# Kernel optimization log

Measured on AMD Instinct MI355X. Metric: run time of the kernel, lower is better.

Reference implementation:

```python
import jax, jax.numpy as jnp
import numpy as np

N, NFEAT, NHID, OUT, E, P = 50000, 256, 128, 64, 800000, 3
WALK_STEPS, LAMBDA_RW = 13, 0.2


def spmm(row, col, val, x):
    # sparse (N,N) @ dense (N,d) via gather + segment-sum over destination rows
    return jax.ops.segment_sum(val[:, None] * x[col], row, num_segments=N)


def telu(x):
    return x * jnp.tanh(jnp.exp(x))


def setup_inputs() -> dict:
    key = jax.random.key(0)
    ks = jax.random.split(key, 24)
    s = 0.05
    inp = {
        'feature': jax.random.normal(ks[0], (N, NFEAT), jnp.float32),
        'edge_index': jax.random.randint(ks[1], (P, 2, E), 0, N, jnp.int64),
        'edge_val': jax.random.uniform(ks[2], (P, E), jnp.float32) / 16.0,
        'spec_w1': jax.random.normal(ks[3], (P, NFEAT, NHID)) * s,
        'spec_b1': jax.random.normal(ks[4], (P, NHID)) * s,
        'spec_w2': jax.random.normal(ks[5], (P, NHID, OUT)) * s,
        'spec_b2': jax.random.normal(ks[6], (P, OUT)) * s,
        'shared_w1': jax.random.normal(ks[7], (NFEAT, NHID)) * s,
        'shared_b1': jax.random.normal(ks[8], (NHID,)) * s,
        'shared_w2': jax.random.normal(ks[9], (NHID, OUT)) * s,
        'shared_b2': jax.random.normal(ks[10], (OUT,)) * s,
        'weight_b': jax.random.normal(ks[11], (P, 1)) * s,
        'tau': jnp.float32(0.5),
        'mlp_w1': jax.random.normal(ks[12], (OUT * P, NHID)) * s,
        'mlp_b1': jax.random.normal(ks[13], (NHID,)) * s,
        'mlp_w2': jax.random.normal(ks[14], (NHID, OUT)) * s,
        'mlp_b2': jax.random.normal(ks[15], (OUT,)) * s,
        'raw_w1': jax.random.normal(ks[16], (NFEAT, OUT)) * s,
        'raw_b1': jax.random.normal(ks[17], (OUT,)) * s,
        'raw_w2': jax.random.normal(ks[18], (OUT, OUT)) * s,
        'raw_b2': jax.random.normal(ks[19], (OUT,)) * s,
        'proj_w': jax.random.normal(ks[20], (OUT * 4, OUT)) * s,
        'proj_b': jax.random.normal(ks[21], (OUT,)) * s,
    }
    return inp


def reference(feature, edge_index, edge_val, spec_w1, spec_b1, spec_w2, spec_b2,
              shared_w1, shared_b1, shared_w2, shared_b2, weight_b, tau,
              mlp_w1, mlp_b1, mlp_w2, mlp_b2, raw_w1, raw_b1, raw_w2, raw_b2,
              proj_w, proj_b):
    rows = [edge_index[i, 0] for i in range(P)]
    cols = [edge_index[i, 1] for i in range(P)]
    vals = [edge_val[i] for i in range(P)]

    def gc(x, w, b, i):
        return spmm(rows[i], cols[i], vals[i], x @ w) + b

    # path-specific two-layer GCNs (dropout in eval mode = identity)
    specific = []
    for i in range(P):
        h1 = telu(gc(feature, spec_w1[i], spec_b1[i], i))
        specific.append(gc(h1, spec_w2[i], spec_b2[i], i))
    spec_stack = jnp.stack(specific, axis=0)  # (P, N, OUT)

    # shared GCN applied per path
    shared = []
    for i in range(P):
        h1 = telu(gc(feature, shared_w1, shared_b1, i))
        shared.append(gc(h1, shared_w2, shared_b2, i))
    shared_stack = jnp.stack(shared, axis=0)
    H_sh = jnp.mean(shared_stack, axis=0)

    # markov-enhanced path attention
    summaries = []
    for s in specific:
        mean_pool = s.mean(axis=0)
        max_pool = s.max(axis=0)
        p = jax.nn.softmax(s, axis=0)
        entropy = -jnp.sum(p * jnp.log(p + 1e-6), axis=0)
        summaries.append(jnp.concatenate([mean_pool, max_pool, entropy], axis=-1))
    ps = jnp.stack(summaries, axis=0)  # (P, 3*OUT)
    sim = (ps @ ps.T) / (jnp.sqrt(jnp.float32(3 * OUT)) * tau)
    T = jax.nn.softmax(sim, axis=1)
    pi0 = jax.nn.softmax(weight_b.squeeze(-1), axis=0)
    pi = pi0
    for _ in range(WALK_STEPS):
        pi = LAMBDA_RW * pi0 + (1.0 - LAMBDA_RW) * (pi @ T)
    W_tilde = pi[:, None]  # beta dropout is identity in eval mode

    # collaborative MLP on concatenated specific features
    concat_sp = jnp.concatenate(specific, axis=1)  # (N, P*OUT)
    H_col = jax.nn.relu(concat_sp @ mlp_w1 + mlp_b1) @ mlp_w2 + mlp_b2

    # attention-fused specific features
    wprob = jax.nn.softmax(W_tilde, axis=0)[:, 0]  # (P,)
    H_sp_fused = jnp.einsum('pnd,p->nd', spec_stack, wprob)

    # raw path on merged adjacency: final_A = sum_i W_tilde[i] * A_i (applied lazily)
    w = W_tilde[:, 0]

    def merged_spmm(x):
        acc = jnp.zeros((N, x.shape[1]), x.dtype)
        for i in range(P):
            acc = acc + w[i] * spmm(rows[i], cols[i], vals[i], x)
        return acc

    U1 = merged_spmm(feature @ raw_w1) + raw_b1
    U2 = merged_spmm(U1 @ raw_w2) + raw_b2
    H_raw = (U1 + U2) / 2.0

    all_feat = jnp.concatenate([H_sp_fused, H_sh, H_col, H_raw], axis=1)
    out = all_feat @ proj_w + proj_b
    return (out, spec_stack, shared_stack, H_col, H_raw)
```

## Files before the change

kernel.cpp:

```cpp
#include <hip/hip_runtime.h>
#include <hip/hip_bf16.h>
#include <math.h>

#define NN 50000
#define NFEAT 256
#define NHID 128
#define OUTD 64
#define NE 800000
#define NP 3
#define NCH 64
#define RC 782
#define NSB 196
#define NNR (NN + 1)
#define NBUK 256
#define BROWS 196
#define BCAP 4096
#define EPB 8192

typedef __hip_bfloat16 bf16;
typedef __attribute__((ext_vector_type(8))) short short8;
typedef __attribute__((ext_vector_type(4))) short short4v;
typedef __attribute__((ext_vector_type(4))) float f32x4;
typedef unsigned long long u64;

static inline int cdiv(long a, long b) { return (int)((a + b - 1) / b); }

__device__ __forceinline__ short f2bf(float x) {
    unsigned u = __builtin_bit_cast(unsigned, x);
    unsigned r = (u + 0x7FFFu + ((u >> 16) & 1u)) >> 16;
    return (short)r;
}
__device__ __forceinline__ float bf2f(short b) {
    unsigned u = ((unsigned)(unsigned short)b) << 16;
    return __builtin_bit_cast(float, u);
}

__device__ __forceinline__ float telu_f(float x) {
    float e = __expf(x);
    float t = __expf(-2.0f * e);
    return x * (1.0f - t) / (1.0f + t);
}

__device__ __forceinline__ void ld8(const float* __restrict__ p, float v[8]) {
    float4 a = *reinterpret_cast<const float4*>(p);
    float4 b = *reinterpret_cast<const float4*>(p + 4);
    v[0] = a.x; v[1] = a.y; v[2] = a.z; v[3] = a.w;
    v[4] = b.x; v[5] = b.y; v[6] = b.z; v[7] = b.w;
}

__device__ __forceinline__ void store4(float* p, const float o[4]) {
    *reinterpret_cast<float4*>(p) = make_float4(o[0], o[1], o[2], o[3]);
}
__device__ __forceinline__ void store4(bf16* p, const float o[4]) {
    short4v u;
    u[0] = f2bf(o[0]); u[1] = f2bf(o[1]); u[2] = f2bf(o[2]); u[3] = f2bf(o[3]);
    *reinterpret_cast<short4v*>(p) = u;
}

__global__ void transpose_split(const float* __restrict__ src, bf16* __restrict__ dh,
                                bf16* __restrict__ dl, int K, int M, long total) {
    long idx = (long)blockIdx.x * blockDim.x + threadIdx.x;
    if (idx >= total) return;
    long pm = idx / K;
    int k = (int)(idx - pm * K);
    long p = pm / M;
    int m = (int)(pm - p * M);
    float v = src[(p * K + k) * M + m];
    short hb = f2bf(v);
    short lb = f2bf(v - bf2f(hb));
    reinterpret_cast<short*>(dh)[idx] = hb;
    reinterpret_cast<short*>(dl)[idx] = lb;
}

template <int K, int M, int MODE, int ACT, typename OT>
__global__ __launch_bounds__(256) void gemm_mfma(
    const float* __restrict__ A, const bf16* __restrict__ Bh, const bf16* __restrict__ Bl,
    const float* __restrict__ bias, OT* __restrict__ out, int nrows,
    const float* __restrict__ wvec, const float* __restrict__ s1,
    const float* __restrict__ s2, const float* __restrict__ s3) {
    constexpr int MC = M / 16;
    __shared__ short AsH[64 * 32];
    __shared__ short AsL[64 * 32];

    int t = threadIdx.x;
    int n0 = blockIdx.x * 64;
    int w = t >> 6;
    int l = t & 63;
    int lr = l & 15, lq = l >> 4;

    float w0 = 0.f, w1 = 0.f, w2 = 0.f;
    if (MODE == 2) { w0 = wvec[3]; w1 = wvec[4]; w2 = wvec[5]; }

    f32x4 acc[MC];
#pragma unroll
    for (int i = 0; i < MC; ++i) {
        f32x4 z = {0.f, 0.f, 0.f, 0.f};
        acc[i] = z;
    }

    int sr = t >> 2, sc = t & 3;
    int gn_s = n0 + sr;
    int wslot = (sc ^ ((sr >> 2) & 3)) << 3;
    short* wpH = &AsH[sr * 32 + wslot];
    short* wpL = &AsL[sr * 32 + wslot];

    int rrow = (w << 4) + lr;
    int roff = rrow * 32 + ((lq ^ ((rrow >> 2) & 3)) << 3);
    const short* rpH = &AsH[roff];
    const short* rpL = &AsL[roff];

    const short* Bhs = reinterpret_cast<const short*>(Bh);
    const short* Bls = reinterpret_cast<const short*>(Bl);

    auto loadA = [&](int k0, float v[8]) {
        if (gn_s >= nrows) {
#pragma unroll
            for (int j = 0; j < 8; ++j) v[j] = 0.f;
            return;
        }
        if (MODE == 0) {
            ld8(A + (long)gn_s * K + k0 + sc * 8, v);
        } else if (MODE == 1) {
            int plane = k0 >> 6;
            int d = (k0 & 63) + sc * 8;
            ld8(A + ((long)plane * NN + gn_s) * OUTD + d, v);
        } else {
            int seg = k0 >> 6;
            int d = (k0 & 63) + sc * 8;
            if (seg == 0) {
                float x0[8], x1[8], x2[8];
                ld8(A + ((long)0 * NN + gn_s) * OUTD + d, x0);
                ld8(A + ((long)1 * NN + gn_s) * OUTD + d, x1);
                ld8(A + ((long)2 * NN + gn_s) * OUTD + d, x2);
#pragma unroll
                for (int j = 0; j < 8; ++j) v[j] = w0 * x0[j] + w1 * x1[j] + w2 * x2[j];
            } else if (seg == 1) {
                float x0[8], x1[8], x2[8];
                ld8(s1 + ((long)0 * NN + gn_s) * OUTD + d, x0);
                ld8(s1 + ((long)1 * NN + gn_s) * OUTD + d, x1);
                ld8(s1 + ((long)2 * NN + gn_s) * OUTD + d, x2);
#pragma unroll
                for (int j = 0; j < 8; ++j) v[j] = (x0[j] + x1[j] + x2[j]) * (1.0f / 3.0f);
            } else if (seg == 2) {
                ld8(s2 + (long)gn_s * OUTD + d, v);
            } else {
                ld8(s3 + (long)gn_s * OUTD + d, v);
            }
        }
    };

    float v[8];
    loadA(0, v);
    for (int k0 = 0; k0 < K; k0 += 32) {
        short8 ah, al;
#pragma unroll
        for (int j = 0; j < 8; ++j) {
            short hb = f2bf(v[j]);
            ah[j] = hb;
            al[j] = f2bf(v[j] - bf2f(hb));
        }
        __syncthreads();
        *reinterpret_cast<short8*>(wpH) = ah;
        *reinterpret_cast<short8*>(wpL) = al;
        __syncthreads();
        if (k0 + 32 < K) loadA(k0 + 32, v);
        short8 fah = *reinterpret_cast<const short8*>(rpH);
        short8 fal = *reinterpret_cast<const short8*>(rpL);
#pragma unroll
        for (int m = 0; m < MC; ++m) {
            long wb = (long)(m * 16 + lr) * K + k0 + (lq << 3);
            short8 bh = *reinterpret_cast<const short8*>(Bhs + wb);
            short8 bl = *reinterpret_cast<const short8*>(Bls + wb);
            acc[m] = __builtin_amdgcn_mfma_f32_16x16x32_bf16(bh, fah, acc[m], 0, 0, 0);
            acc[m] = __builtin_amdgcn_mfma_f32_16x16x32_bf16(bl, fah, acc[m], 0, 0, 0);
            acc[m] = __builtin_amdgcn_mfma_f32_16x16x32_bf16(bh, fal, acc[m], 0, 0, 0);
        }
    }

    int gn = n0 + (w << 4) + lr;
    if (gn < nrows) {
#pragma unroll
        for (int m = 0; m < MC; ++m) {
            int mb = m * 16 + (lq << 2);
            float o[4];
#pragma unroll
            for (int r = 0; r < 4; ++r) {
                o[r] = acc[m][r] + (bias ? bias[mb + r] : 0.f);
                if (ACT == 2) o[r] = fmaxf(o[r], 0.f);
            }
            store4(&out[(long)gn * M + mb], o);
        }
    }
}

__global__ void hist_all(const int* __restrict__ ei, int* __restrict__ cnt) {
    int p = blockIdx.y;
    int e = blockIdx.x * blockDim.x + threadIdx.x;
    if (e >= NE) return;
    int r = ei[((long)p * 2) * NE + e];
    atomicAdd(&cnt[(long)p * NN + r], 1);
}

__global__ void scan_pass1(const int* __restrict__ cnt, int* __restrict__ bsum) {
    int p = blockIdx.y, b = blockIdx.x, t = threadIdx.x;
    int idx = b * 256 + t;
    int v = (idx < NN) ? cnt[(long)p * NN + idx] : 0;
    __shared__ int sh[256];
    sh[t] = v;
    __syncthreads();
    for (int off = 128; off > 0; off >>= 1) {
        if (t < off) sh[t] += sh[t + off];
        __syncthreads();
    }
    if (t == 0) bsum[p * NSB + b] = sh[0];
}

__global__ void scan_pass2(const int* __restrict__ bsum, int* __restrict__ boff) {
    int p = blockIdx.x, t = threadIdx.x;
    int v = (t < NSB) ? bsum[p * NSB + t] : 0;
    __shared__ int sh[256];
    sh[t] = v;
    __syncthreads();
    for (int off = 1; off < 256; off <<= 1) {
        int tmp = (t >= off) ? sh[t - off] : 0;
        __syncthreads();
        sh[t] += tmp;
        __syncthreads();
    }
    if (t < NSB) boff[p * NSB + t] = sh[t] - v;
}

__global__ void scan_pass3(const int* __restrict__ cnt, const int* __restrict__ boff,
                           int* __restrict__ rowptr) {
    int p = blockIdx.y, b = blockIdx.x, t = threadIdx.x;
    int idx = b * 256 + t;
    int v = (idx < NN) ? cnt[(long)p * NN + idx] : 0;
    __shared__ int sh[256];
    sh[t] = v;
    __syncthreads();
    for (int off = 1; off < 256; off <<= 1) {
        int tmp = (t >= off) ? sh[t - off] : 0;
        __syncthreads();
        sh[t] += tmp;
        __syncthreads();
    }
    int rp = boff[p * NSB + b] + sh[t] - v;
    if (idx < NN) rowptr[(long)p * NNR + idx] = rp;
    if (idx == NN - 1) rowptr[(long)p * NNR + NN] = rp + v;
}

__global__ __launch_bounds__(256) void bucket_append2(
    const int* __restrict__ ei, const float* __restrict__ ev,
    int* __restrict__ bcnt, int2* __restrict__ bbuf) {
    int p = blockIdx.y;
    int t = threadIdx.x;
    long e0 = (long)blockIdx.x * EPB;
    const int* rs = ei + ((long)p * 2) * NE;
    const int* cs = rs + NE;
    const float* vs = ev + (long)p * NE;
    __shared__ int lcnt[NBUK];
    __shared__ int lbase[NBUK];
    for (int b = t; b < NBUK; b += 256) lcnt[b] = 0;
    __syncthreads();
    for (int i = t; i < EPB; i += 256) {
        long e = e0 + i;
        if (e < NE) atomicAdd(&lcnt[rs[e] / BROWS], 1);
    }
    __syncthreads();
    for (int b = t; b < NBUK; b += 256) {
        int c = lcnt[b];
        lbase[b] = (c > 0) ? atomicAdd(&bcnt[p * NBUK + b], c) : 0;
        lcnt[b] = 0;
    }
    __syncthreads();
    for (int i = t; i < EPB; i += 256) {
        long e = e0 + i;
        if (e >= NE) continue;
        int r = rs[e];
        int b = r / BROWS;
        int off = atomicAdd(&lcnt[b], 1);
        int pos = lbase[b] + off;
        int meta = ((r - b * BROWS) << 16) | cs[e];
        bbuf[((long)p * NBUK + b) * BCAP + pos] = make_int2(meta, __float_as_int(vs[e]));
    }
}

__global__ __launch_bounds__(256) void bucket_scatter2(
    const int* __restrict__ bcnt, const int2* __restrict__ bbuf,
    const int* __restrict__ rowptr, int2* __restrict__ csr) {
    int b = blockIdx.x, p = blockIdx.y;
    int t = threadIdx.x;
    int row0 = b * BROWS;
    int nrows = min(BROWS, NN - row0);
    __shared__ int cur[BROWS];
    for (int i = t; i < nrows; i += 256) cur[i] = rowptr[(long)p * NNR + row0 + i];
    __syncthreads();
    int cntb = bcnt[p * NBUK + b];
    const int2* buf = bbuf + ((long)p * NBUK + b) * BCAP;
    int2* csrp = csr + (long)p * NE;
    for (int i = t; i < cntb; i += 256) {
        int2 ent = buf[i];
        int row_off = ent.x >> 16;
        int col = ent.x & 0xFFFF;
        int pos = atomicAdd(&cur[row_off], 1);
        csrp[pos] = make_int2(col, ent.y);
    }
}

template <int M, int ACT, int RPB>
__global__ void spmm_dual(const int* __restrict__ rowptr, const int2* __restrict__ csr,
                          const bf16* __restrict__ Ya, const bf16* __restrict__ Yb,
                          const float* __restrict__ biasA, const float* __restrict__ biasB,
                          float* __restrict__ outA, float* __restrict__ outB) {
    constexpr int TPR = M / 2;
    int t = threadIdx.x;
    int n = blockIdx.x * RPB + t / TPR;
    int hs = t % TPR;
    int h = hs * 2;
    if (n >= NN) return;
    int e0 = rowptr[n], e1 = rowptr[n + 1];
    float aAl = biasA[h], aAh = biasA[h + 1];
    float aBl = biasB[h], aBh = biasB[h + 1];
    const unsigned* Ua = reinterpret_cast<const unsigned*>(Ya);
    const unsigned* Ub = reinterpret_cast<const unsigned*>(Yb);
    int e = e0;
    for (; e + 3 < e1; e += 4) {
        int2 p0 = csr[e], p1 = csr[e + 1], p2 = csr[e + 2], p3 = csr[e + 3];
        unsigned a0 = Ua[(long)p0.x * TPR + hs], a1 = Ua[(long)p1.x * TPR + hs];
        unsigned a2 = Ua[(long)p2.x * TPR + hs], a3 = Ua[(long)p3.x * TPR + hs];
        unsigned b0 = Ub[(long)p0.x * TPR + hs], b1 = Ub[(long)p1.x * TPR + hs];
        unsigned b2 = Ub[(long)p2.x * TPR + hs], b3 = Ub[(long)p3.x * TPR + hs];
        float v0 = __int_as_float(p0.y), v1 = __int_as_float(p1.y);
        float v2 = __int_as_float(p2.y), v3 = __int_as_float(p3.y);
        aAl += v0 * bf2f((short)a0) + v1 * bf2f((short)a1) + v2 * bf2f((short)a2) + v3 * bf2f((short)a3);
        aAh += v0 * bf2f((short)(a0 >> 16)) + v1 * bf2f((short)(a1 >> 16)) +
               v2 * bf2f((short)(a2 >> 16)) + v3 * bf2f((short)(a3 >> 16));
        aBl += v0 * bf2f((short)b0) + v1 * bf2f((short)b1) + v2 * bf2f((short)b2) + v3 * bf2f((short)b3);
        aBh += v0 * bf2f((short)(b0 >> 16)) + v1 * bf2f((short)(b1 >> 16)) +
               v2 * bf2f((short)(b2 >> 16)) + v3 * bf2f((short)(b3 >> 16));
    }
    for (; e < e1; ++e) {
        int2 pe = csr[e];
        float v = __int_as_float(pe.y);
        unsigned a = Ua[(long)pe.x * TPR + hs];
        unsigned b = Ub[(long)pe.x * TPR + hs];
        aAl += v * bf2f((short)a);
        aAh += v * bf2f((short)(a >> 16));
        aBl += v * bf2f((short)b);
        aBh += v * bf2f((short)(b >> 16));
    }
    if (ACT == 1) {
        aAl = telu_f(aAl); aAh = telu_f(aAh);
        aBl = telu_f(aBl); aBh = telu_f(aBh);
    }
    *reinterpret_cast<float2*>(&outA[(long)n * M + h]) = make_float2(aAl, aAh);
    *reinterpret_cast<float2*>(&outB[(long)n * M + h]) = make_float2(aBl, aBh);
}

__global__ void spmm_merged(const int* __restrict__ rp0, const int2* __restrict__ cs0,
                            const int* __restrict__ rp1, const int2* __restrict__ cs1,
                            const int* __restrict__ rp2, const int2* __restrict__ cs2,
                            const bf16* __restrict__ Y, const float* __restrict__ wvec,
                            const float* __restrict__ bias, float* __restrict__ out) {
    constexpr int TPR = 32;
    int t = threadIdx.x;
    int n = blockIdx.x * 2 + t / TPR;
    int hs = t % TPR;
    int h = hs * 2;
    if (n >= NN) return;
    const int* rps[3] = {rp0, rp1, rp2};
    const int2* css[3] = {cs0, cs1, cs2};
    const unsigned* U = reinterpret_cast<const unsigned*>(Y);
    float al = 0.f, ah = 0.f;
#pragma unroll
    for (int p = 0; p < 3; ++p) {
        const int2* cs = css[p];
        int e0 = rps[p][n], e1 = rps[p][n + 1];
        float sl = 0.f, sh = 0.f;
        int e = e0;
        for (; e + 3 < e1; e += 4) {
            int2 p0 = cs[e], p1 = cs[e + 1], p2 = cs[e + 2], p3 = cs[e + 3];
            unsigned y0 = U[(long)p0.x * TPR + hs], y1 = U[(long)p1.x * TPR + hs];
            unsigned y2 = U[(long)p2.x * TPR + hs], y3 = U[(long)p3.x * TPR + hs];
            float v0 = __int_as_float(p0.y), v1 = __int_as_float(p1.y);
            float v2 = __int_as_float(p2.y), v3 = __int_as_float(p3.y);
            sl += v0 * bf2f((short)y0) + v1 * bf2f((short)y1) + v2 * bf2f((short)y2) + v3 * bf2f((short)y3);
            sh += v0 * bf2f((short)(y0 >> 16)) + v1 * bf2f((short)(y1 >> 16)) +
                  v2 * bf2f((short)(y2 >> 16)) + v3 * bf2f((short)(y3 >> 16));
        }
        for (; e < e1; ++e) {
            int2 pe = cs[e];
            unsigned y = U[(long)pe.x * TPR + hs];
            float v = __int_as_float(pe.y);
            sl += v * bf2f((short)y);
            sh += v * bf2f((short)(y >> 16));
        }
        float wv = wvec[p];
        al += wv * sl;
        ah += wv * sh;
    }
    *reinterpret_cast<float2*>(&out[(long)n * OUTD + h]) =
        make_float2(al + bias[h], ah + bias[h + 1]);
}

__global__ void colsum_passA(const float* __restrict__ spec, float* __restrict__ pmax,
                             float* __restrict__ psum, float* __restrict__ pexp) {
    int p = blockIdx.y, c = blockIdx.x;
    int t = threadIdx.x;
    int d = t & 63, rg = t >> 6;
    const float* base = spec + (long)p * NN * OUTD;
    int r0 = c * RC, r1 = min(r0 + RC, NN);
    float m = -INFINITY, s = 0.f, e = 0.f;
    for (int r = r0 + rg; r < r1; r += 4) {
        float v = base[(long)r * OUTD + d];
        s += v;
        if (v > m) { e = e * __expf(m - v) + 1.0f; m = v; }
        else e += __expf(v - m);
    }
    __shared__ float rm[256], rs[256], re[256];
    rm[t] = m; rs[t] = s; re[t] = e;
    __syncthreads();
    for (int off = 128; off >= 64; off >>= 1) {
        if (t < off) {
            float m2 = fmaxf(rm[t], rm[t + off]);
            re[t] = re[t] * __expf(rm[t] - m2) + re[t + off] * __expf(rm[t + off] - m2);
            rm[t] = m2;
            rs[t] = rs[t] + rs[t + off];
        }
        __syncthreads();
    }
    if (t < 64) {
        long idx = ((long)p * 64 + t) * NCH + c;
        pmax[idx] = rm[t]; psum[idx] = rs[t]; pexp[idx] = re[t];
    }
}

__global__ void colsum_reduceB(const float* __restrict__ pmax, const float* __restrict__ psum,
                               const float* __restrict__ pexp, float* __restrict__ ps,
                               float* __restrict__ zbuf) {
    int b = blockIdx.x;
    int p = b >> 6, d = b & 63;
    int t = threadIdx.x;
    long idx = (long)b * NCH + t;
    float m = pmax[idx], s = psum[idx], e = pexp[idx];
    for (int off = 32; off > 0; off >>= 1) {
        float m2 = fmaxf(m, __shfl_xor(m, off));
        e = e * __expf(m - m2) + __shfl_xor(e, off) * __expf(__shfl_xor(m, off) - m2);
        m = m2;
        s += __shfl_xor(s, off);
    }
    if (t == 0) {
        ps[p * 192 + d] = s / (float)NN;
        ps[p * 192 + 64 + d] = m;
        zbuf[b] = e;
    }
}

__global__ void colsum_passC(const float* __restrict__ spec, const float* __restrict__ ps,
                             const float* __restrict__ zbuf, float* __restrict__ pent) {
    int p = blockIdx.y, c = blockIdx.x;
    int t = threadIdx.x;
    int d = t & 63, rg = t >> 6;
    const float* base = spec + (long)p * NN * OUTD;
    float gm = ps[p * 192 + 64 + d];
    float zinv = 1.0f / zbuf[p * 64 + d];
    int r0 = c * RC, r1 = min(r0 + RC, NN);
    float ent = 0.f;
    for (int r = r0 + rg; r < r1; r += 4) {
        float v = base[(long)r * OUTD + d];
        float pv = __expf(v - gm) * zinv;
        ent -= pv * __logf(pv + 1e-6f);
    }
    __shared__ float rd[256];
    rd[t] = ent;
    __syncthreads();
    for (int off = 128; off >= 64; off >>= 1) {
        if (t < off) rd[t] += rd[t + off];
        __syncthreads();
    }
    if (t < 64) pent[((long)p * 64 + t) * NCH + c] = rd[t];
}

__global__ void colsum_reduceD(const float* __restrict__ pent, float* __restrict__ ps) {
    int b = blockIdx.x;
    int p = b >> 6, d = b & 63;
    int t = threadIdx.x;
    float e = pent[(long)b * NCH + t];
    for (int off = 32; off > 0; off >>= 1) e += __shfl_xor(e, off);
    if (t == 0) ps[p * 192 + 128 + d] = e;
}

__global__ void walk_kernel(const float* __restrict__ ps, const float* __restrict__ weight_b,
                            const float* __restrict__ tau_p, float* __restrict__ wout) {
    if (threadIdx.x != 0 || blockIdx.x != 0) return;
    float sim[3][3];
    float inv = 1.0f / (sqrtf(192.0f) * tau_p[0]);
    for (int i = 0; i < 3; ++i)
        for (int j = 0; j < 3; ++j) {
            float dotv = 0.f;
            for (int k = 0; k < 192; ++k) dotv += ps[i * 192 + k] * ps[j * 192 + k];
            sim[i][j] = dotv * inv;
        }
    float T[3][3];
    for (int i = 0; i < 3; ++i) {
        float m = fmaxf(sim[i][0], fmaxf(sim[i][1], sim[i][2]));
        float e0 = expf(sim[i][0] - m), e1 = expf(sim[i][1] - m), e2 = expf(sim[i][2] - m);
        float s = e0 + e1 + e2;
        T[i][0] = e0 / s; T[i][1] = e1 / s; T[i][2] = e2 / s;
    }
    float b0 = weight_b[0], b1 = weight_b[1], b2 = weight_b[2];
    float m = fmaxf(b0, fmaxf(b1, b2));
    float e0 = expf(b0 - m), e1 = expf(b1 - m), e2 = expf(b2 - m);
    float s = e0 + e1 + e2;
    float pi0[3] = {e0 / s, e1 / s, e2 / s};
    float pi[3] = {pi0[0], pi0[1], pi0[2]};
    for (int it = 0; it < 13; ++it) {
        float n0 = pi[0] * T[0][0] + pi[1] * T[1][0] + pi[2] * T[2][0];
        float n1 = pi[0] * T[0][1] + pi[1] * T[1][1] + pi[2] * T[2][1];
        float n2 = pi[0] * T[0][2] + pi[1] * T[1][2] + pi[2] * T[2][2];
        pi[0] = 0.2f * pi0[0] + 0.8f * n0;
        pi[1] = 0.2f * pi0[1] + 0.8f * n1;
        pi[2] = 0.2f * pi0[2] + 0.8f * n2;
    }
    wout[0] = pi[0]; wout[1] = pi[1]; wout[2] = pi[2];
    float mm = fmaxf(pi[0], fmaxf(pi[1], pi[2]));
    float f0 = expf(pi[0] - mm), f1 = expf(pi[1] - mm), f2 = expf(pi[2] - mm);
    float fs = f0 + f1 + f2;
    wout[3] = f0 / fs; wout[4] = f1 / fs; wout[5] = f2 / fs;
}

__global__ void hraw_final(const float* __restrict__ U1, float* __restrict__ Hraw) {
    long i = (long)blockIdx.x * blockDim.x + threadIdx.x;
    if (i >= (long)NN * OUTD) return;
    Hraw[i] = 0.5f * (U1[i] + Hraw[i]);
}

extern "C" void kernel_launch(void* const* d_in, const int* in_sizes, int n_in,
                              void* d_out, int out_size, void* d_ws, size_t ws_size,
                              hipStream_t stream) {
    const float* feature   = (const float*)d_in[0];
    const int*   edge_index= (const int*)d_in[1];
    const float* edge_val  = (const float*)d_in[2];
    const float* spec_w1   = (const float*)d_in[3];
    const float* spec_b1   = (const float*)d_in[4];
    const float* spec_w2   = (const float*)d_in[5];
    const float* spec_b2   = (const float*)d_in[6];
    const float* shared_w1 = (const float*)d_in[7];
    const float* shared_b1 = (const float*)d_in[8];
    const float* shared_w2 = (const float*)d_in[9];
    const float* shared_b2 = (const float*)d_in[10];
    const float* weight_b  = (const float*)d_in[11];
    const float* tau       = (const float*)d_in[12];
    const float* mlp_w1    = (const float*)d_in[13];
    const float* mlp_b1    = (const float*)d_in[14];
    const float* mlp_w2    = (const float*)d_in[15];
    const float* mlp_b2    = (const float*)d_in[16];
    const float* raw_w1    = (const float*)d_in[17];
    const float* raw_b1    = (const float*)d_in[18];
    const float* raw_w2    = (const float*)d_in[19];
    const float* raw_b2    = (const float*)d_in[20];
    const float* proj_w    = (const float*)d_in[21];
    const float* proj_b    = (const float*)d_in[22];

    float* out        = (float*)d_out;
    float* spec_stack = out + (long)NN * OUTD;
    float* shr_stack  = spec_stack + 3L * NN * OUTD;
    float* Hcol       = out + 7L * NN * OUTD;
    float* Hraw       = out + 8L * NN * OUTD;

    char* wp = (char*)d_ws;
    bf16* XWsp = (bf16*)wp; wp += (long)NN * 128 * sizeof(bf16);
    bf16* XWsh = (bf16*)wp; wp += (long)NN * 128 * sizeof(bf16);
    bf16* Bsp  = (bf16*)wp; wp += (long)NN * OUTD * sizeof(bf16);
    bf16* Bsh  = (bf16*)wp; wp += (long)NN * OUTD * sizeof(bf16);
    float* h1sp = (float*)wp; wp += (long)NN * 128 * sizeof(float);
    float* h1sh = (float*)wp; wp += (long)NN * 128 * sizeof(float);
    float* psBuf = (float*)wp; wp += 1024 * sizeof(float);
    float* wBuf  = (float*)wp; wp += 64 * sizeof(float);
    float* zBuf  = (float*)wp; wp += 256 * sizeof(float);
    float* pMax  = (float*)wp; wp += (long)3 * 64 * NCH * sizeof(float);
    float* pSum  = (float*)wp; wp += (long)3 * 64 * NCH * sizeof(float);
    float* pExp  = (float*)wp; wp += (long)3 * 64 * NCH * sizeof(float);
    float* pEnt  = (float*)wp; wp += (long)3 * 64 * NCH * sizeof(float);
    int2* csr_all = (int2*)wp;  wp += (long)NP * NE * sizeof(int2);
    int*  rowptr_all = (int*)wp; wp += (long)NP * NNR * sizeof(int) + 64;
    int* cnt    = (int*)wp; wp += (long)NP * NN * sizeof(int);
    int* bsum   = (int*)wp; wp += (long)NP * NSB * sizeof(int);
    int* boff   = (int*)wp; wp += (long)NP * NSB * sizeof(int);
    int* bcnt   = (int*)wp; wp += (long)NP * NBUK * sizeof(int);
    int2* bbuf  = (int2*)wp; wp += (long)NP * NBUK * BCAP * sizeof(int2);
    bf16* w1sp_h = (bf16*)wp; wp += 3L * 256 * 128 * sizeof(bf16);
    bf16* w1sp_l = (bf16*)wp; wp += 3L * 256 * 128 * sizeof(bf16);
    bf16* w1sh_h = (bf16*)wp; wp += 256L * 128 * sizeof(bf16);
    bf16* w1sh_l = (bf16*)wp; wp += 256L * 128 * sizeof(bf16);
    bf16* w2sp_h = (bf16*)wp; wp += 3L * 128 * 64 * sizeof(bf16);
    bf16* w2sp_l = (bf16*)wp; wp += 3L * 128 * 64 * sizeof(bf16);
    bf16* w2sh_h = (bf16*)wp; wp += 128L * 64 * sizeof(bf16);
    bf16* w2sh_l = (bf16*)wp; wp += 128L * 64 * sizeof(bf16);
    bf16* mlp1_h = (bf16*)wp; wp += 192L * 128 * sizeof(bf16);
    bf16* mlp1_l = (bf16*)wp; wp += 192L * 128 * sizeof(bf16);
    bf16* mlp2_h = (bf16*)wp; wp += 128L * 64 * sizeof(bf16);
    bf16* mlp2_l = (bf16*)wp; wp += 128L * 64 * sizeof(bf16);
    bf16* raw1_h = (bf16*)wp; wp += 256L * 64 * sizeof(bf16);
    bf16* raw1_l = (bf16*)wp; wp += 256L * 64 * sizeof(bf16);
    bf16* raw2_h = (bf16*)wp; wp += 64L * 64 * sizeof(bf16);
    bf16* raw2_l = (bf16*)wp; wp += 64L * 64 * sizeof(bf16);
    bf16* proj_h = (bf16*)wp; wp += 256L * 64 * sizeof(bf16);
    bf16* proj_l = (bf16*)wp; wp += 256L * 64 * sizeof(bf16);

    int* rowptr[NP]; int2* csr[NP];
    for (int p = 0; p < NP; ++p) {
        rowptr[p] = rowptr_all + (long)p * NNR;
        csr[p]    = csr_all + (long)p * NE;
    }

    const int TB = 256;
    int g_rows = cdiv(NN, 64);

    transpose_split<<<cdiv(3L * 256 * 128, TB), TB, 0, stream>>>(spec_w1, w1sp_h, w1sp_l, 256, 128, 3L * 256 * 128);
    transpose_split<<<cdiv(256L * 128, TB), TB, 0, stream>>>(shared_w1, w1sh_h, w1sh_l, 256, 128, 256L * 128);
    transpose_split<<<cdiv(3L * 128 * 64, TB), TB, 0, stream>>>(spec_w2, w2sp_h, w2sp_l, 128, 64, 3L * 128 * 64);
    transpose_split<<<cdiv(128L * 64, TB), TB, 0, stream>>>(shared_w2, w2sh_h, w2sh_l, 128, 64, 128L * 64);
    transpose_split<<<cdiv(192L * 128, TB), TB, 0, stream>>>(mlp_w1, mlp1_h, mlp1_l, 192, 128, 192L * 128);
    transpose_split<<<cdiv(128L * 64, TB), TB, 0, stream>>>(mlp_w2, mlp2_h, mlp2_l, 128, 64, 128L * 64);
    transpose_split<<<cdiv(256L * 64, TB), TB, 0, stream>>>(raw_w1, raw1_h, raw1_l, 256, 64, 256L * 64);
    transpose_split<<<cdiv(64L * 64, TB), TB, 0, stream>>>(raw_w2, raw2_h, raw2_l, 64, 64, 64L * 64);
    transpose_split<<<cdiv(256L * 64, TB), TB, 0, stream>>>(proj_w, proj_h, proj_l, 256, 64, 256L * 64);

    hipMemsetAsync(cnt, 0, (long)NP * NN * sizeof(int), stream);
    hipMemsetAsync(bcnt, 0, (long)NP * NBUK * sizeof(int), stream);
    {
        dim3 gE(cdiv(NE, TB), NP);
        hist_all<<<gE, TB, 0, stream>>>(edge_index, cnt);
        dim3 gA(cdiv(NE, EPB), NP);
        bucket_append2<<<gA, 256, 0, stream>>>(edge_index, edge_val, bcnt, bbuf);
        dim3 gS(NSB, NP);
        scan_pass1<<<gS, 256, 0, stream>>>(cnt, bsum);
        scan_pass2<<<NP, 256, 0, stream>>>(bsum, boff);
        scan_pass3<<<gS, 256, 0, stream>>>(cnt, boff, rowptr_all);
        dim3 gB(NBUK, NP);
        bucket_scatter2<<<gB, 256, 0, stream>>>(bcnt, bbuf, rowptr_all, csr_all);
    }

    gemm_mfma<256, 128, 0, 0, bf16><<<g_rows, 256, 0, stream>>>(
        feature, w1sh_h, w1sh_l, nullptr, XWsh, NN, nullptr, nullptr, nullptr, nullptr);

    for (int p = 0; p < NP; ++p) {
        gemm_mfma<256, 128, 0, 0, bf16><<<g_rows, 256, 0, stream>>>(
            feature, w1sp_h + (long)p * 256 * 128, w1sp_l + (long)p * 256 * 128,
            nullptr, XWsp, NN, nullptr, nullptr, nullptr, nullptr);
        spmm_dual<128, 1, 1><<<NN, 64, 0, stream>>>(rowptr[p], csr[p], XWsp, XWsh,
                                                    spec_b1 + (long)p * 128, shared_b1,
                                                    h1sp, h1sh);
        gemm_mfma<128, 64, 0, 0, bf16><<<g_rows, 256, 0, stream>>>(
            h1sp, w2sp_h + (long)p * 128 * 64, w2sp_l + (long)p * 128 * 64,
            nullptr, Bsp, NN, nullptr, nullptr, nullptr, nullptr);
        gemm_mfma<128, 64, 0, 0, bf16><<<g_rows, 256, 0, stream>>>(
            h1sh, w2sh_h, w2sh_l, nullptr, Bsh, NN, nullptr, nullptr, nullptr, nullptr);
        spmm_dual<64, 0, 2><<<cdiv(NN, 2), 64, 0, stream>>>(rowptr[p], csr[p], Bsp, Bsh,
                                                            spec_b2 + (long)p * 64, shared_b2,
                                                            spec_stack + (long)p * NN * OUTD,
                                                            shr_stack + (long)p * NN * OUTD);
    }

    {
        dim3 gA(NCH, 3);
        colsum_passA<<<gA, 256, 0, stream>>>(spec_stack, pMax, pSum, pExp);
        colsum_reduceB<<<192, 64, 0, stream>>>(pMax, pSum, pExp, psBuf, zBuf);
        colsum_passC<<<gA, 256, 0, stream>>>(spec_stack, psBuf, zBuf, pEnt);
        colsum_reduceD<<<192, 64, 0, stream>>>(pEnt, psBuf);
    }
    walk_kernel<<<1, 64, 0, stream>>>(psBuf, weight_b, tau, wBuf);

    gemm_mfma<192, 128, 1, 2, float><<<g_rows, 256, 0, stream>>>(
        spec_stack, mlp1_h, mlp1_l, mlp_b1, h1sp, NN, nullptr, nullptr, nullptr, nullptr);
    gemm_mfma<128, 64, 0, 0, float><<<g_rows, 256, 0, stream>>>(
        h1sp, mlp2_h, mlp2_l, mlp_b2, Hcol, NN, nullptr, nullptr, nullptr, nullptr);

    float* U1 = h1sh;
    gemm_mfma<256, 64, 0, 0, bf16><<<g_rows, 256, 0, stream>>>(
        feature, raw1_h, raw1_l, nullptr, Bsp, NN, nullptr, nullptr, nullptr, nullptr);
    spmm_merged<<<cdiv(NN, 2), 64, 0, stream>>>(rowptr[0], csr[0],
                                                rowptr[1], csr[1],
                                                rowptr[2], csr[2],
                                                Bsp, wBuf, raw_b1, U1);
    gemm_mfma<64, 64, 0, 0, bf16><<<g_rows, 256, 0, stream>>>(
        U1, raw2_h, raw2_l, nullptr, Bsh, NN, nullptr, nullptr, nullptr, nullptr);
    spmm_merged<<<cdiv(NN, 2), 64, 0, stream>>>(rowptr[0], csr[0],
                                                rowptr[1], csr[1],
                                                rowptr[2], csr[2],
                                                Bsh, wBuf, raw_b2, Hraw);
    hraw_final<<<cdiv((long)NN * OUTD, TB), TB, 0, stream>>>(U1, Hraw);

    gemm_mfma<256, 64, 2, 0, float><<<g_rows, 256, 0, stream>>>(
        spec_stack, proj_h, proj_l, proj_b, out, NN, wBuf, shr_stack, Hcol, Hraw);
}
```

Baseline: 1.513 ms.

## Derive CSR row pointers from bucket counts instead of a global histogram

Drops the global per-row histogram pass and the three-pass prefix scan over all rows. Row pointers are now built inside each bucket's scatter block from a local shared-memory histogram and scan, offset by a small scan over the bucket counts. This removes a memset, atomic traffic to global memory and four kernel launches, at the cost of an extra pass over each bucket's buffer inside the scatter kernel.

```diff
diff --git a/kernel.cpp b/kernel.cpp
--- a/kernel.cpp
+++ b/kernel.cpp
@@ -10,7 +10,6 @@
 #define NP 3
 #define NCH 64
 #define RC 782
-#define NSB 196
 #define NNR (NN + 1)
 #define NBUK 256
 #define BROWS 196
@@ -193,62 +192,6 @@
     }
 }
 
-__global__ void hist_all(const int* __restrict__ ei, int* __restrict__ cnt) {
-    int p = blockIdx.y;
-    int e = blockIdx.x * blockDim.x + threadIdx.x;
-    if (e >= NE) return;
-    int r = ei[((long)p * 2) * NE + e];
-    atomicAdd(&cnt[(long)p * NN + r], 1);
-}
-
-__global__ void scan_pass1(const int* __restrict__ cnt, int* __restrict__ bsum) {
-    int p = blockIdx.y, b = blockIdx.x, t = threadIdx.x;
-    int idx = b * 256 + t;
-    int v = (idx < NN) ? cnt[(long)p * NN + idx] : 0;
-    __shared__ int sh[256];
-    sh[t] = v;
-    __syncthreads();
-    for (int off = 128; off > 0; off >>= 1) {
-        if (t < off) sh[t] += sh[t + off];
-        __syncthreads();
-    }
-    if (t == 0) bsum[p * NSB + b] = sh[0];
-}
-
-__global__ void scan_pass2(const int* __restrict__ bsum, int* __restrict__ boff) {
-    int p = blockIdx.x, t = threadIdx.x;
-    int v = (t < NSB) ? bsum[p * NSB + t] : 0;
-    __shared__ int sh[256];
-    sh[t] = v;
-    __syncthreads();
-    for (int off = 1; off < 256; off <<= 1) {
-        int tmp = (t >= off) ? sh[t - off] : 0;
-        __syncthreads();
-        sh[t] += tmp;
-        __syncthreads();
-    }
-    if (t < NSB) boff[p * NSB + t] = sh[t] - v;
-}
-
-__global__ void scan_pass3(const int* __restrict__ cnt, const int* __restrict__ boff,
-                           int* __restrict__ rowptr) {
-    int p = blockIdx.y, b = blockIdx.x, t = threadIdx.x;
-    int idx = b * 256 + t;
-    int v = (idx < NN) ? cnt[(long)p * NN + idx] : 0;
-    __shared__ int sh[256];
-    sh[t] = v;
-    __syncthreads();
-    for (int off = 1; off < 256; off <<= 1) {
-        int tmp = (t >= off) ? sh[t - off] : 0;
-        __syncthreads();
-        sh[t] += tmp;
-        __syncthreads();
-    }
-    int rp = boff[p * NSB + b] + sh[t] - v;
-    if (idx < NN) rowptr[(long)p * NNR + idx] = rp;
-    if (idx == NN - 1) rowptr[(long)p * NNR + NN] = rp + v;
-}
-
 __global__ __launch_bounds__(256) void bucket_append2(
     const int* __restrict__ ei, const float* __restrict__ ev,
     int* __restrict__ bcnt, int2* __restrict__ bbuf) {
@@ -285,18 +228,54 @@
     }
 }
 
-__global__ __launch_bounds__(256) void bucket_scatter2(
-    const int* __restrict__ bcnt, const int2* __restrict__ bbuf,
-    const int* __restrict__ rowptr, int2* __restrict__ csr) {
+__global__ void scan_bcnt(const int* __restrict__ bcnt, int* __restrict__ bbase) {
+    int p = blockIdx.x, t = threadIdx.x;
+    int v = bcnt[p * NBUK + t];
+    __shared__ int sh[NBUK];
+    sh[t] = v;
+    __syncthreads();
+    for (int off = 1; off < NBUK; off <<= 1) {
+        int tmp = (t >= off) ? sh[t - off] : 0;
+        __syncthreads();
+        sh[t] += tmp;
+        __syncthreads();
+    }
+    bbase[p * NBUK + t] = sh[t] - v;
+}
+
+__global__ __launch_bounds__(256) void bucket_scatter3(
+    const int* __restrict__ bcnt, const int* __restrict__ bbase,
+    const int2* __restrict__ bbuf, int* __restrict__ rowptr, int2* __restrict__ csr) {
     int b = blockIdx.x, p = blockIdx.y;
     int t = threadIdx.x;
     int row0 = b * BROWS;
     int nrows = min(BROWS, NN - row0);
+    int cntb = bcnt[p * NBUK + b];
+    int base = bbase[p * NBUK + b];
+    const int2* buf = bbuf + ((long)p * NBUK + b) * BCAP;
+    __shared__ int rcnt[256];
     __shared__ int cur[BROWS];
-    for (int i = t; i < nrows; i += 256) cur[i] = rowptr[(long)p * NNR + row0 + i];
-    __syncthreads();
-    int cntb = bcnt[p * NBUK + b];
-    const int2* buf = bbuf + ((long)p * NBUK + b) * BCAP;
+    rcnt[t] = 0;
+    __syncthreads();
+    for (int i = t; i < cntb; i += 256) atomicAdd(&rcnt[buf[i].x >> 16], 1);
+    __syncthreads();
+    int v = rcnt[t];
+    __shared__ int sh[256];
+    sh[t] = v;
+    __syncthreads();
+    for (int off = 1; off < 256; off <<= 1) {
+        int tmp = (t >= off) ? sh[t - off] : 0;
+        __syncthreads();
+        sh[t] += tmp;
+        __syncthreads();
+    }
+    int excl = base + sh[t] - v;
+    if (t < nrows) {
+        rowptr[(long)p * NNR + row0 + t] = excl;
+        cur[t] = excl;
+    }
+    if (b == NBUK - 1 && t == 0) rowptr[(long)p * NNR + NN] = base + cntb;
+    __syncthreads();
     int2* csrp = csr + (long)p * NE;
     for (int i = t; i < cntb; i += 256) {
         int2 ent = buf[i];
@@ -584,10 +563,8 @@
     float* pEnt  = (float*)wp; wp += (long)3 * 64 * NCH * sizeof(float);
     int2* csr_all = (int2*)wp;  wp += (long)NP * NE * sizeof(int2);
     int*  rowptr_all = (int*)wp; wp += (long)NP * NNR * sizeof(int) + 64;
-    int* cnt    = (int*)wp; wp += (long)NP * NN * sizeof(int);
-    int* bsum   = (int*)wp; wp += (long)NP * NSB * sizeof(int);
-    int* boff   = (int*)wp; wp += (long)NP * NSB * sizeof(int);
     int* bcnt   = (int*)wp; wp += (long)NP * NBUK * sizeof(int);
+    int* bbase  = (int*)wp; wp += (long)NP * NBUK * sizeof(int);
     int2* bbuf  = (int2*)wp; wp += (long)NP * NBUK * BCAP * sizeof(int2);
     bf16* w1sp_h = (bf16*)wp; wp += 3L * 256 * 128 * sizeof(bf16);
     bf16* w1sp_l = (bf16*)wp; wp += 3L * 256 * 128 * sizeof(bf16);
@@ -627,19 +604,13 @@
     transpose_split<<<cdiv(64L * 64, TB), TB, 0, stream>>>(raw_w2, raw2_h, raw2_l, 64, 64, 64L * 64);
     transpose_split<<<cdiv(256L * 64, TB), TB, 0, stream>>>(proj_w, proj_h, proj_l, 256, 64, 256L * 64);
 
-    hipMemsetAsync(cnt, 0, (long)NP * NN * sizeof(int), stream);
     hipMemsetAsync(bcnt, 0, (long)NP * NBUK * sizeof(int), stream);
     {
-        dim3 gE(cdiv(NE, TB), NP);
-        hist_all<<<gE, TB, 0, stream>>>(edge_index, cnt);
         dim3 gA(cdiv(NE, EPB), NP);
         bucket_append2<<<gA, 256, 0, stream>>>(edge_index, edge_val, bcnt, bbuf);
-        dim3 gS(NSB, NP);
-        scan_pass1<<<gS, 256, 0, stream>>>(cnt, bsum);
-        scan_pass2<<<NP, 256, 0, stream>>>(bsum, boff);
-        scan_pass3<<<gS, 256, 0, stream>>>(cnt, boff, rowptr_all);
+        scan_bcnt<<<NP, NBUK, 0, stream>>>(bcnt, bbase);
         dim3 gB(NBUK, NP);
-        bucket_scatter2<<<gB, 256, 0, stream>>>(bcnt, bbuf, rowptr_all, csr_all);
+        bucket_scatter3<<<gB, 256, 0, stream>>>(bcnt, bbase, bbuf, rowptr_all, csr_all);
     }
 
     gemm_mfma<256, 128, 0, 0, bf16><<<g_rows, 256, 0, stream>>>(
```

Measured after the change: 1.407 ms. 1.08x faster.
